# Kernel optimization log

Measured on AMD Instinct MI355X. Metric: run time of the kernel, lower is better.

## Reference

```python
import jax, jax.numpy as jnp
import numpy as np

N_NODES = 20000
N_EDGES = 320000
IN_CH = 256
HID_CH = 512


def setup_inputs() -> dict:
    key = jax.random.key(0)
    k_x, k_e, k_w1, k_w2 = jax.random.split(key, 4)
    x = jax.random.normal(k_x, (N_NODES, IN_CH), dtype=jnp.float32)
    edge_index = jax.random.randint(k_e, (2, N_EDGES), 0, N_NODES, dtype=jnp.int32)
    # Glorot-style init for the two GCNConv weight matrices; PyG GCNConv bias init is zeros.
    W1 = jax.random.normal(k_w1, (IN_CH, HID_CH), dtype=jnp.float32) * (1.0 / np.sqrt(IN_CH))
    b1 = jnp.zeros((HID_CH,), dtype=jnp.float32)
    W2 = jax.random.normal(k_w2, (HID_CH, HID_CH), dtype=jnp.float32) * (1.0 / np.sqrt(HID_CH))
    b2 = jnp.zeros((HID_CH,), dtype=jnp.float32)
    return {"x": x, "edge_index": edge_index, "W1": W1, "b1": b1, "W2": W2, "b2": b2}


def _gcn_conv(x, W, b, src, dst, n_nodes):
    """PyG GCNConv: linear transform, then sym-normalized aggregation with self-loops."""
    h = x @ W  # [N, H]
    # in-degree on dst, +1 for the implicit self-loop
    deg = jnp.zeros((n_nodes,), dtype=h.dtype).at[dst].add(1.0) + 1.0
    dinv = jax.lax.rsqrt(deg)  # deg >= 1 always
    norm = dinv[src] * dinv[dst]  # [E]
    msg = h[src] * norm[:, None]  # [E, H] gathered, normalized messages
    agg = jax.ops.segment_sum(msg, dst, num_segments=n_nodes)  # scatter-add to targets
    # self-loop contribution: norm for edge i->i is dinv[i]^2
    return agg + h * (dinv * dinv)[:, None] + b


def reference(x, edge_index, W1, b1, W2, b2):
    src, dst = edge_index[0], edge_index[1]
    n = x.shape[0]
    h = jax.nn.relu(_gcn_conv(x, W1, b1, src, dst, n))
    # dropout(p=0.2) is identity in eval mode
    return _gcn_conv(h, W2, b2, src, dst, n)
```

## Files before the change

kernel.cpp:

```cpp
#include <hip/hip_runtime.h>

#define N_NODES 20000
#define N_EDGES 320000
#define IN_CH 256
#define HID_CH 512
#define NB_SCAN ((N_NODES + 255) / 256)
#define EB ((N_EDGES + 255) / 256)

typedef unsigned short u16;
typedef __attribute__((ext_vector_type(4))) float f32x4;
typedef __attribute__((ext_vector_type(8))) short bf16x8;
typedef __attribute__((ext_vector_type(4))) u16 u16x4;
typedef __attribute__((ext_vector_type(8))) u16 u16x8;

__device__ __forceinline__ float bf2f(u16 h) { return __uint_as_float((unsigned)h << 16); }
__device__ __forceinline__ u16 f2bf(float f) {
    unsigned u = __float_as_uint(f);
    return (u16)((u + 0x7fffu + ((u >> 16) & 1u)) >> 16);
}

__global__ void zero_kernel(int* __restrict__ deg, int* __restrict__ cursor,
                            int* __restrict__ flag, int n, int nf) {
    int i = blockIdx.x * blockDim.x + threadIdx.x;
    if (i < n) { deg[i] = 0; cursor[i] = 0; }
    if (i < nf) flag[i] = 0;
}

__global__ __launch_bounds__(256) void count_convert_kernel(
        const int* __restrict__ dst, int* __restrict__ deg,
        const float* __restrict__ x, u16* __restrict__ xb,
        const float* __restrict__ W1, u16* __restrict__ hi1,
        const float* __restrict__ W2, u16* __restrict__ hi2) {
    __shared__ float t[64][65];
    int b = blockIdx.x;
    if (b < EB) {
        int i = b * 256 + threadIdx.x;
        if (i < N_EDGES) atomicAdd(&deg[dst[i]], 1);
        return;
    }
    b -= EB;
    const int XB = N_NODES * IN_CH / 4 / 256;
    if (b < XB) {
        int i = b * 256 + threadIdx.x;
        float4 v = ((const float4*)x)[i];
        u16x4 o = {f2bf(v.x), f2bf(v.y), f2bf(v.z), f2bf(v.w)};
        ((u16x4*)xb)[i] = o;
        return;
    }
    b -= XB;
    const float* W;
    u16* hi;
    int K;
    if (b < 32) { W = W1; hi = hi1; K = IN_CH; }
    else        { b -= 32; W = W2; hi = hi2; K = HID_CH; }
    const int N = HID_CH;
    int k0 = (b >> 3) * 64, n0 = (b & 7) * 64;
    int c = threadIdx.x & 63, r4 = threadIdx.x >> 6;
#pragma unroll
    for (int i = 0; i < 16; ++i) {
        int r = i * 4 + r4;
        t[r][c] = W[(size_t)(k0 + r) * N + n0 + c];
    }
    __syncthreads();
#pragma unroll
    for (int i = 0; i < 16; ++i) {
        int n = i * 4 + r4;
        hi[(size_t)(n0 + n) * K + k0 + c] = f2bf(t[c][n]);
    }
}

__global__ __launch_bounds__(256) void scan_one_kernel(
        const int* __restrict__ deg, float* __restrict__ dinv, int* __restrict__ row_ptr,
        int* __restrict__ agg, int* __restrict__ flag, int N, int E) {
    __shared__ int tmp[256];
    __shared__ int part[256];
    int t = threadIdx.x, b = blockIdx.x;
    int i = b * 256 + t;
    int d = (i < N) ? deg[i] : 0;
    if (i < N) dinv[i] = rsqrtf((float)d + 1.0f);
    tmp[t] = d;
    __syncthreads();
#pragma unroll
    for (int off = 1; off < 256; off <<= 1) {
        int v = (t >= off) ? tmp[t - off] : 0;
        __syncthreads();
        tmp[t] += v;
        __syncthreads();
    }
    if (t == 255) {
        __hip_atomic_store(&agg[b], tmp[255], __ATOMIC_RELAXED, __HIP_MEMORY_SCOPE_AGENT);
        __hip_atomic_store(&flag[b], 1, __ATOMIC_RELEASE, __HIP_MEMORY_SCOPE_AGENT);
    }
    int v = 0;
    if (t < b) {
        while (__hip_atomic_load(&flag[t], __ATOMIC_ACQUIRE, __HIP_MEMORY_SCOPE_AGENT) == 0) {
            __builtin_amdgcn_s_sleep(8);
        }
        v = __hip_atomic_load(&agg[t], __ATOMIC_RELAXED, __HIP_MEMORY_SCOPE_AGENT);
    }
    part[t] = v;
    __syncthreads();
#pragma unroll
    for (int off = 128; off > 0; off >>= 1) {
        if (t < off) part[t] += part[t + off];
        __syncthreads();
    }
    int base = part[0];
    if (i < N) row_ptr[i] = base + tmp[t] - d;
    if (i == 0) row_ptr[N] = E;
}

__global__ void scatter_edges_kernel(const int* __restrict__ src, const int* __restrict__ dst,
                                     const int* __restrict__ row_ptr, int* __restrict__ cursor,
                                     const float* __restrict__ dinv, int2* __restrict__ epair,
                                     int E) {
    int e = blockIdx.x * blockDim.x + threadIdx.x;
    if (e >= E) return;
    int d = dst[e];
    int s = src[e];
    int pos = row_ptr[d] + atomicAdd(&cursor[d], 1);
    epair[pos] = make_int2(s, __float_as_int(dinv[s]));
}

template <int C, int SLICES>
__global__ __launch_bounds__(256) void gather_agg_kernel(
        const u16* __restrict__ h, const int2* __restrict__ epair,
        const int* __restrict__ row_ptr, const float* __restrict__ dinv,
        u16* __restrict__ z, int N) {
    int bid = blockIdx.x;
    int nb, s;
    if (SLICES == 8) {
        nb = bid >> 3;
        s = bid & 7;
    } else {
        nb = (bid >> 3) * 2 + (bid & 1);
        s = (bid & 7) >> 1;
    }
    int t = threadIdx.x;
    int grp = t >> 3;
    int u = t & 7;
    int n = nb * 32 + grp;
    bool alive = (n < N);
    int nn = alive ? n : (N - 1);
    float dn = dinv[nn];
    const u16* hbase = h + s * 64 + u * 8;
    float acc[8];
    {
        u16x8 ws = *(const u16x8*)(hbase + (size_t)nn * C);
        float sf = dn * dn;
#pragma unroll
        for (int j = 0; j < 8; ++j) acc[j] = bf2f(ws[j]) * sf;
    }
    int e0 = row_ptr[nn];
    int e1 = alive ? row_ptr[nn + 1] : e0;
    int e = e0;
    for (; e + 8 <= e1; e += 8) {
        int2 p[8];
        u16x8 w[8];
#pragma unroll
        for (int b = 0; b < 8; ++b) p[b] = epair[e + b];
#pragma unroll
        for (int b = 0; b < 8; ++b) w[b] = *(const u16x8*)(hbase + (size_t)p[b].x * C);
#pragma unroll
        for (int b = 0; b < 8; ++b) {
            float nr = __int_as_float(p[b].y) * dn;
#pragma unroll
            for (int j = 0; j < 8; ++j) acc[j] = fmaf(bf2f(w[b][j]), nr, acc[j]);
        }
    }
    for (; e + 4 <= e1; e += 4) {
        int2 p0 = epair[e + 0], p1 = epair[e + 1], p2 = epair[e + 2], p3 = epair[e + 3];
        u16x8 w0 = *(const u16x8*)(hbase + (size_t)p0.x * C);
        u16x8 w1 = *(const u16x8*)(hbase + (size_t)p1.x * C);
        u16x8 w2 = *(const u16x8*)(hbase + (size_t)p2.x * C);
        u16x8 w3 = *(const u16x8*)(hbase + (size_t)p3.x * C);
        float n0 = __int_as_float(p0.y) * dn, n1 = __int_as_float(p1.y) * dn;
        float n2 = __int_as_float(p2.y) * dn, n3 = __int_as_float(p3.y) * dn;
#pragma unroll
        for (int j = 0; j < 8; ++j) {
            acc[j] = fmaf(bf2f(w0[j]), n0, acc[j]);
            acc[j] = fmaf(bf2f(w1[j]), n1, acc[j]);
            acc[j] = fmaf(bf2f(w2[j]), n2, acc[j]);
            acc[j] = fmaf(bf2f(w3[j]), n3, acc[j]);
        }
    }
    for (; e < e1; ++e) {
        int2 p = epair[e];
        u16x8 w = *(const u16x8*)(hbase + (size_t)p.x * C);
        float nr = __int_as_float(p.y) * dn;
#pragma unroll
        for (int j = 0; j < 8; ++j) acc[j] = fmaf(bf2f(w[j]), nr, acc[j]);
    }
    if (alive) {
        u16x8 vh;
#pragma unroll
        for (int j = 0; j < 8; ++j) vh[j] = f2bf(acc[j]);
        *(u16x8*)(z + (size_t)n * C + s * 64 + u * 8) = vh;
    }
}

template <int K, bool RELU, bool OUT_BF16>
__global__ __launch_bounds__(512, 8) void gemm_mfma_kernel(
        const u16* __restrict__ A, const u16* __restrict__ Bh,
        const float* __restrict__ bias, void* __restrict__ Cout, int M, int N) {
    __shared__ u16 lds[2][8192];
    const int tid = threadIdx.x;
    const int lane = tid & 63;
    const int wid = tid >> 6;

    const int nmt = (M + 127) / 128;
    const int total = nmt * 4;
    int bid = blockIdx.x;
    int q = total >> 3, r = total & 7;
    int xcd = bid & 7, pp = bid >> 3;
    int lin = (xcd < r) ? (xcd * (q + 1) + pp) : (r * (q + 1) + (xcd - r) * q + pp);
    const int bm = (lin >> 2) * 128;
    const int bn = (lin & 3) * 128;

    const int wm = (wid & 1) * 64;
    const int wn = (wid >> 1) * 32;

    f32x4 acc[4][2];
#pragma unroll
    for (int i = 0; i < 4; ++i)
#pragma unroll
        for (int j = 0; j < 2; ++j) acc[i][j] = (f32x4){0.f, 0.f, 0.f, 0.f};

    const int srow = (wid << 4) + (lane >> 2);
    const int scb = (((lane & 3) ^ ((lane >> 3) & 3)) << 4);
    const char* srcA  = (const char*)(A  + (size_t)min(bm + srow, M - 1) * K) + scb;
    const char* srcBh = (const char*)(Bh + (size_t)(bn + srow) * K) + scb;
    const int dstoff = wid << 10;

#define GLL(srcp, dstb)                                                                  \
    __builtin_amdgcn_global_load_lds(                                                    \
        (const __attribute__((address_space(1))) void*)(srcp),                           \
        (__attribute__((address_space(3))) void*)((char*)&lds[buf][0] + (dstb)), 16, 0, 0)

#define STAGE(bufv, k0)                                                                  \
    do {                                                                                 \
        int buf = (bufv);                                                                \
        size_t kb2 = (size_t)(k0) * 2;                                                   \
        GLL(srcA + kb2, dstoff);                                                         \
        GLL(srcBh + kb2, 8192 + dstoff);                                                 \
    } while (0)

    STAGE(0, 0);

    const int NT = K / 32;
    const int kb = (lane >> 4) << 4;
#pragma unroll
    for (int t = 0; t < NT; ++t) {
        int cur = t & 1;
        if (t + 1 < NT) {
            STAGE(cur ^ 1, (t + 1) * 32);
            asm volatile("s_waitcnt vmcnt(2)" ::: "memory");
        } else {
            asm volatile("s_waitcnt vmcnt(0)" ::: "memory");
        }
        __builtin_amdgcn_s_barrier();
        asm volatile("" ::: "memory");

        const char* L = (const char*)&lds[cur][0];
        bf16x8 a[4], b_h[2];
#pragma unroll
        for (int i = 0; i < 4; ++i) {
            int ra = wm + i * 16 + (lane & 15);
            int off = ra * 64 + (kb ^ (((ra >> 1) & 3) << 4));
            a[i] = *(const bf16x8*)(L + off);
        }
#pragma unroll
        for (int j = 0; j < 2; ++j) {
            int rb = wn + j * 16 + (lane & 15);
            int off = rb * 64 + (kb ^ (((rb >> 1) & 3) << 4));
            b_h[j] = *(const bf16x8*)(L + 8192 + off);
        }
#pragma unroll
        for (int i = 0; i < 4; ++i)
#pragma unroll
            for (int j = 0; j < 2; ++j)
                acc[i][j] = __builtin_amdgcn_mfma_f32_16x16x32_bf16(a[i], b_h[j], acc[i][j], 0, 0, 0);
        asm volatile("" ::: "memory");
        __builtin_amdgcn_s_barrier();
    }
#undef STAGE
#undef GLL

#pragma unroll
    for (int j = 0; j < 2; ++j) {
        int gc = bn + wn + j * 16 + (lane & 15);
        float bv = bias[gc];
#pragma unroll
        for (int i = 0; i < 4; ++i) {
#pragma unroll
            for (int t = 0; t < 4; ++t) {
                int gr = bm + wm + i * 16 + ((lane >> 4) << 2) + t;
                if (gr < M) {
                    float v = acc[i][j][t] + bv;
                    if (RELU) v = fmaxf(v, 0.f);
                    if (OUT_BF16)
                        ((u16*)Cout)[(size_t)gr * N + gc] = f2bf(v);
                    else
                        ((float*)Cout)[(size_t)gr * N + gc] = v;
                }
            }
        }
    }
}

extern "C" void kernel_launch(void* const* d_in, const int* in_sizes, int n_in,
                              void* d_out, int out_size, void* d_ws, size_t ws_size,
                              hipStream_t stream) {
    const float* x  = (const float*)d_in[0];
    const int*   ei = (const int*)d_in[1];
    const float* W1 = (const float*)d_in[2];
    const float* b1 = (const float*)d_in[3];
    const float* W2 = (const float*)d_in[4];
    const float* b2 = (const float*)d_in[5];
    const int* src = ei;
    const int* dst = ei + N_EDGES;

    char* ws = (char*)d_ws;
    size_t off = 0;
    auto alloc = [&](size_t bytes) {
        void* p = ws + off;
        off = (off + bytes + 255) & ~(size_t)255;
        return p;
    };
    int*   deg     = (int*)alloc(N_NODES * 4);
    int*   cursor  = (int*)alloc(N_NODES * 4);
    int*   row_ptr = (int*)alloc((N_NODES + 1) * 4);
    float* dinv    = (float*)alloc(N_NODES * 4);
    int*   agg     = (int*)alloc(NB_SCAN * 4);
    int*   flag    = (int*)alloc(NB_SCAN * 4);
    int2*  epair   = (int2*)alloc((size_t)N_EDGES * 8);
    u16*   wt1_hi  = (u16*)alloc((size_t)IN_CH * HID_CH * 2);
    u16*   wt2_hi  = (u16*)alloc((size_t)HID_CH * HID_CH * 2);
    u16*   xb      = (u16*)alloc((size_t)N_NODES * IN_CH * 2);
    u16*   z1      = (u16*)alloc((size_t)N_NODES * IN_CH * 2);
    u16*   z2      = (u16*)alloc((size_t)N_NODES * HID_CH * 2);
    u16*   h1      = (u16*)d_out;

    zero_kernel<<<NB_SCAN, 256, 0, stream>>>(deg, cursor, flag, N_NODES, NB_SCAN);
    const int XB = N_NODES * IN_CH / 4 / 256;
    count_convert_kernel<<<EB + XB + 96, 256, 0, stream>>>(dst, deg, x, xb, W1, wt1_hi, W2,
                                                           wt2_hi);
    scan_one_kernel<<<NB_SCAN, 256, 0, stream>>>(deg, dinv, row_ptr, agg, flag, N_NODES,
                                                 N_EDGES);
    scatter_edges_kernel<<<EB, 256, 0, stream>>>(src, dst, row_ptr, cursor, dinv, epair,
                                                 N_EDGES);

    const int NMT = (N_NODES + 127) / 128;
    const int NB32 = (N_NODES + 31) / 32;
    gather_agg_kernel<IN_CH, 4><<<((NB32 + 1) / 2) * 8, 256, 0, stream>>>(
        xb, epair, row_ptr, dinv, z1, N_NODES);
    gemm_mfma_kernel<IN_CH, true, true><<<NMT * 4, 512, 0, stream>>>(z1, wt1_hi, b1, h1,
                                                                     N_NODES, HID_CH);

    gather_agg_kernel<HID_CH, 8><<<NB32 * 8, 256, 0, stream>>>(
        h1, epair, row_ptr, dinv, z2, N_NODES);
    gemm_mfma_kernel<HID_CH, false, false><<<NMT * 4, 512, 0, stream>>>(z2, wt2_hi, b2,
                                                                        (float*)d_out, N_NODES,
                                                                        HID_CH);
}
```

Measured before the change: 149.8 us.

## Fuse CSR build and conversions into one cooperative grid-synced kernel

Replaces four preprocessing launches (zero, count/convert, decoupled-lookback scan, edge scatter) with a single cooperative kernel of 256 blocks that uses grid.sync between phases. This removes launch gaps and the spin-wait flag protocol. In exchange it runs the work on a fixed 256-block grid with grid-stride loops and pays the cost of several grid-wide barriers, which may reduce parallelism for the edge and conversion phases.

```diff
diff --git a/kernel.cpp b/kernel.cpp
--- a/kernel.cpp
+++ b/kernel.cpp
@@ -1,11 +1,13 @@
 #include <hip/hip_runtime.h>
+#include <hip/hip_cooperative_groups.h>
+
+namespace cg = cooperative_groups;
 
 #define N_NODES 20000
 #define N_EDGES 320000
 #define IN_CH 256
 #define HID_CH 512
 #define NB_SCAN ((N_NODES + 255) / 256)
-#define EB ((N_EDGES + 255) / 256)
 
 typedef unsigned short u16;
 typedef __attribute__((ext_vector_type(4))) float f32x4;
@@ -19,107 +21,98 @@
     return (u16)((u + 0x7fffu + ((u >> 16) & 1u)) >> 16);
 }
 
-__global__ void zero_kernel(int* __restrict__ deg, int* __restrict__ cursor,
-                            int* __restrict__ flag, int n, int nf) {
-    int i = blockIdx.x * blockDim.x + threadIdx.x;
-    if (i < n) { deg[i] = 0; cursor[i] = 0; }
-    if (i < nf) flag[i] = 0;
-}
-
-__global__ __launch_bounds__(256) void count_convert_kernel(
-        const int* __restrict__ dst, int* __restrict__ deg,
+__global__ __launch_bounds__(256) void csr_coop_kernel(
+        const int* __restrict__ src, const int* __restrict__ dst,
+        int* __restrict__ deg, int* __restrict__ cursor, float* __restrict__ dinv,
+        int* __restrict__ row_ptr, int* __restrict__ agg, int2* __restrict__ epair,
         const float* __restrict__ x, u16* __restrict__ xb,
         const float* __restrict__ W1, u16* __restrict__ hi1,
         const float* __restrict__ W2, u16* __restrict__ hi2) {
-    __shared__ float t[64][65];
-    int b = blockIdx.x;
-    if (b < EB) {
-        int i = b * 256 + threadIdx.x;
-        if (i < N_EDGES) atomicAdd(&deg[dst[i]], 1);
-        return;
-    }
-    b -= EB;
-    const int XB = N_NODES * IN_CH / 4 / 256;
-    if (b < XB) {
-        int i = b * 256 + threadIdx.x;
+    cg::grid_group grid = cg::this_grid();
+    __shared__ float tS[64][65];
+    int* tmp  = (int*)&tS[0][0];
+    int* part = ((int*)&tS[0][0]) + 256;
+    const int tid = threadIdx.x;
+    const int bid = blockIdx.x;
+    const int gtid = bid * 256 + tid;
+    const int GSZ = 256 * 256;
+
+    for (int i = gtid; i < N_NODES; i += GSZ) { deg[i] = 0; cursor[i] = 0; }
+    for (int i = gtid; i < N_NODES * IN_CH / 4; i += GSZ) {
         float4 v = ((const float4*)x)[i];
         u16x4 o = {f2bf(v.x), f2bf(v.y), f2bf(v.z), f2bf(v.w)};
         ((u16x4*)xb)[i] = o;
-        return;
-    }
-    b -= XB;
-    const float* W;
-    u16* hi;
-    int K;
-    if (b < 32) { W = W1; hi = hi1; K = IN_CH; }
-    else        { b -= 32; W = W2; hi = hi2; K = HID_CH; }
-    const int N = HID_CH;
-    int k0 = (b >> 3) * 64, n0 = (b & 7) * 64;
-    int c = threadIdx.x & 63, r4 = threadIdx.x >> 6;
-#pragma unroll
-    for (int i = 0; i < 16; ++i) {
-        int r = i * 4 + r4;
-        t[r][c] = W[(size_t)(k0 + r) * N + n0 + c];
-    }
-    __syncthreads();
-#pragma unroll
-    for (int i = 0; i < 16; ++i) {
-        int n = i * 4 + r4;
-        hi[(size_t)(n0 + n) * K + k0 + c] = f2bf(t[c][n]);
-    }
-}
-
-__global__ __launch_bounds__(256) void scan_one_kernel(
-        const int* __restrict__ deg, float* __restrict__ dinv, int* __restrict__ row_ptr,
-        int* __restrict__ agg, int* __restrict__ flag, int N, int E) {
-    __shared__ int tmp[256];
-    __shared__ int part[256];
-    int t = threadIdx.x, b = blockIdx.x;
-    int i = b * 256 + t;
-    int d = (i < N) ? deg[i] : 0;
-    if (i < N) dinv[i] = rsqrtf((float)d + 1.0f);
-    tmp[t] = d;
-    __syncthreads();
-#pragma unroll
-    for (int off = 1; off < 256; off <<= 1) {
-        int v = (t >= off) ? tmp[t - off] : 0;
+    }
+    for (int tile = bid; tile < 96; tile += 256) {
+        const float* W;
+        u16* hi;
+        int K, tt = tile;
+        if (tt < 32) { W = W1; hi = hi1; K = IN_CH; }
+        else         { tt -= 32; W = W2; hi = hi2; K = HID_CH; }
+        int k0 = (tt >> 3) * 64, n0 = (tt & 7) * 64;
+        int c = tid & 63, r4 = tid >> 6;
+#pragma unroll
+        for (int i = 0; i < 16; ++i) {
+            int r = i * 4 + r4;
+            tS[r][c] = W[(size_t)(k0 + r) * HID_CH + n0 + c];
+        }
         __syncthreads();
-        tmp[t] += v;
+#pragma unroll
+        for (int i = 0; i < 16; ++i) {
+            int n = i * 4 + r4;
+            hi[(size_t)(n0 + n) * K + k0 + c] = f2bf(tS[c][n]);
+        }
         __syncthreads();
     }
-    if (t == 255) {
-        __hip_atomic_store(&agg[b], tmp[255], __ATOMIC_RELAXED, __HIP_MEMORY_SCOPE_AGENT);
-        __hip_atomic_store(&flag[b], 1, __ATOMIC_RELEASE, __HIP_MEMORY_SCOPE_AGENT);
-    }
-    int v = 0;
-    if (t < b) {
-        while (__hip_atomic_load(&flag[t], __ATOMIC_ACQUIRE, __HIP_MEMORY_SCOPE_AGENT) == 0) {
-            __builtin_amdgcn_s_sleep(8);
-        }
-        v = __hip_atomic_load(&agg[t], __ATOMIC_RELAXED, __HIP_MEMORY_SCOPE_AGENT);
-    }
-    part[t] = v;
-    __syncthreads();
-#pragma unroll
-    for (int off = 128; off > 0; off >>= 1) {
-        if (t < off) part[t] += part[t + off];
+    __threadfence();
+    grid.sync();
+
+    for (int e = gtid; e < N_EDGES; e += GSZ) atomicAdd(&deg[dst[e]], 1);
+    __threadfence();
+    grid.sync();
+
+    int dval = 0, incl = 0;
+    if (bid < NB_SCAN) {
+        int i = bid * 256 + tid;
+        dval = (i < N_NODES) ? deg[i] : 0;
+        if (i < N_NODES) dinv[i] = rsqrtf((float)dval + 1.0f);
+        tmp[tid] = dval;
         __syncthreads();
-    }
-    int base = part[0];
-    if (i < N) row_ptr[i] = base + tmp[t] - d;
-    if (i == 0) row_ptr[N] = E;
-}
-
-__global__ void scatter_edges_kernel(const int* __restrict__ src, const int* __restrict__ dst,
-                                     const int* __restrict__ row_ptr, int* __restrict__ cursor,
-                                     const float* __restrict__ dinv, int2* __restrict__ epair,
-                                     int E) {
-    int e = blockIdx.x * blockDim.x + threadIdx.x;
-    if (e >= E) return;
-    int d = dst[e];
-    int s = src[e];
-    int pos = row_ptr[d] + atomicAdd(&cursor[d], 1);
-    epair[pos] = make_int2(s, __float_as_int(dinv[s]));
+#pragma unroll
+        for (int off = 1; off < 256; off <<= 1) {
+            int v = (tid >= off) ? tmp[tid - off] : 0;
+            __syncthreads();
+            tmp[tid] += v;
+            __syncthreads();
+        }
+        incl = tmp[tid];
+        if (tid == 255) agg[bid] = incl;
+    }
+    __threadfence();
+    grid.sync();
+
+    if (bid < NB_SCAN) {
+        part[tid] = (tid < bid) ? agg[tid] : 0;
+        __syncthreads();
+#pragma unroll
+        for (int off = 128; off > 0; off >>= 1) {
+            if (tid < off) part[tid] += part[tid + off];
+            __syncthreads();
+        }
+        int base = part[0];
+        int i = bid * 256 + tid;
+        if (i < N_NODES) row_ptr[i] = base + incl - dval;
+        if (i == 0) row_ptr[N_NODES] = N_EDGES;
+    }
+    __threadfence();
+    grid.sync();
+
+    for (int e = gtid; e < N_EDGES; e += GSZ) {
+        int d = dst[e];
+        int s = src[e];
+        int pos = row_ptr[d] + atomicAdd(&cursor[d], 1);
+        epair[pos] = make_int2(s, __float_as_int(dinv[s]));
+    }
 }
 
 template <int C, int SLICES>
@@ -332,7 +325,6 @@
     int*   row_ptr = (int*)alloc((N_NODES + 1) * 4);
     float* dinv    = (float*)alloc(N_NODES * 4);
     int*   agg     = (int*)alloc(NB_SCAN * 4);
-    int*   flag    = (int*)alloc(NB_SCAN * 4);
     int2*  epair   = (int2*)alloc((size_t)N_EDGES * 8);
     u16*   wt1_hi  = (u16*)alloc((size_t)IN_CH * HID_CH * 2);
     u16*   wt2_hi  = (u16*)alloc((size_t)HID_CH * HID_CH * 2);
@@ -341,14 +333,13 @@
     u16*   z2      = (u16*)alloc((size_t)N_NODES * HID_CH * 2);
     u16*   h1      = (u16*)d_out;
 
-    zero_kernel<<<NB_SCAN, 256, 0, stream>>>(deg, cursor, flag, N_NODES, NB_SCAN);
-    const int XB = N_NODES * IN_CH / 4 / 256;
-    count_convert_kernel<<<EB + XB + 96, 256, 0, stream>>>(dst, deg, x, xb, W1, wt1_hi, W2,
-                                                           wt2_hi);
-    scan_one_kernel<<<NB_SCAN, 256, 0, stream>>>(deg, dinv, row_ptr, agg, flag, N_NODES,
-                                                 N_EDGES);
-    scatter_edges_kernel<<<EB, 256, 0, stream>>>(src, dst, row_ptr, cursor, dinv, epair,
-                                                 N_EDGES);
+    {
+        void* args[] = {(void*)&src, (void*)&dst, (void*)&deg, (void*)&cursor, (void*)&dinv,
+                        (void*)&row_ptr, (void*)&agg, (void*)&epair, (void*)&x, (void*)&xb,
+                        (void*)&W1, (void*)&wt1_hi, (void*)&W2, (void*)&wt2_hi};
+        hipLaunchCooperativeKernel((void*)csr_coop_kernel, dim3(256), dim3(256), args, 0,
+                                   stream);
+    }
 
     const int NMT = (N_NODES + 127) / 128;
     const int NB32 = (N_NODES + 31) / 32;
```

Result: slower. 369.7 us (+146.7%).
